# Kernel tuning notes

Measured on AMD Instinct MI355X. Metric: run time of the kernel, lower is better.

## Reference

```python
import jax, jax.numpy as jnp
import numpy as np


def setup_inputs() -> dict:
    key = jax.random.key(0)
    ks = jax.random.split(key, 8)
    d, h = 1024, 256
    bl, bh = 2048, 2048
    b = bl + bh
    w = lambda k, shp: jax.random.normal(k, shp, jnp.float32) * 0.02
    return {
        "z_low": jax.random.normal(ks[0], (bl, d), jnp.float32),
        "z_high": jax.random.normal(ks[1], (bh, d), jnp.float32),
        "z_bar": jax.random.normal(ks[2], (b, d), jnp.float32),
        "z_normal": jax.random.normal(ks[3], (b, d), jnp.float32),
        "Wa1": w(ks[4], (d, h)), "ba1": jnp.zeros((h,), jnp.float32),
        "Wa2": w(ks[5], (h,)), "ba2": jnp.zeros((), jnp.float32),
        "W0": w(ks[6], (d, d)), "b0": jnp.zeros((d,), jnp.float32),
        "W1": w(ks[7], (d, d)), "b1": jnp.zeros((d,), jnp.float32),
    }


def _scores(x, Wa1, ba1, Wa2, ba2):
    # Linear -> tanh -> Linear(->1); returns per-row attention logits [N]
    return jnp.tanh(x @ Wa1 + ba1) @ Wa2 + ba2


def _integrate(x, Wa1, ba1, Wa2, ba2):
    a = jax.nn.softmax(_scores(x, Wa1, ba1, Wa2, ba2))  # [N]
    return a @ x  # [dim]


def _loo_pool(x, Wa1, ba1, Wa2, ba2):
    # batched leave-one-out attention pooling: row i pools over all j != i
    n = x.shape[0]
    s = _scores(x, Wa1, ba1, Wa2, ba2)  # [N]
    S = jnp.broadcast_to(s[None, :], (n, n))
    S = jnp.where(jnp.eye(n, dtype=bool), -jnp.inf, S)
    A = jax.nn.softmax(S, axis=-1)  # [N,N], zero on diagonal
    return A @ x  # [N, dim]


def _cos(a, b, eps=1e-8):
    na = jnp.maximum(jnp.linalg.norm(a, axis=-1), eps)
    nb = jnp.maximum(jnp.linalg.norm(b, axis=-1), eps)
    return jnp.sum(a * b, axis=-1) / (na * nb)


def reference(z_low, z_high, z_bar, z_normal, Wa1, ba1, Wa2, ba2, W0, b0, W1, b1):
    z_all = jnp.concatenate([z_low, z_high], axis=0)  # [B, d]
    batch = z_all.shape[0]

    z_hat = jnp.concatenate([
        _loo_pool(z_low, Wa1, ba1, Wa2, ba2),
        _loo_pool(z_high, Wa1, ba1, Wa2, ba2),
    ], axis=0)  # [B, d]
    z_tumor = _loo_pool(z_all, Wa1, ba1, Wa2, ba2)  # [B, d]
    z_norm = _integrate(z_normal, Wa1, ba1, Wa2, ba2)  # [d]

    lin0 = lambda v: v @ W0 + b0
    lin1 = lambda v: v @ W1 + b1

    base = lin0(z_hat) + lin1(z_bar)
    pred_tumor = base + lin0(z_tumor)          # [B, d]
    pred_normal = base + lin0(z_norm)[None, :]  # [B, d]

    cpc_tumor = z_all @ pred_tumor.T    # [B, B]
    cpc_normal = z_all @ pred_normal.T  # [B, B]
    eye = jnp.eye(batch, dtype=cpc_tumor.dtype)
    total = eye * cpc_tumor + (1.0 - eye) * cpc_normal

    loss_tcl = jnp.sum(jnp.diag(jax.nn.log_softmax(total, axis=1))) / (-1.0 * batch)

    ones = jnp.ones((batch,), z_all.dtype)
    cos_loss = jnp.mean(ones - _cos(z_all, z_hat)) + jnp.mean(ones - _cos(z_all, z_bar))
    hinge_in = _cos(z_all, pred_tumor) - _cos(z_all, pred_normal)
    hinge = jnp.mean(jnp.maximum(0.0, 1.0 - hinge_in))  # HingeEmbeddingLoss, target=-1, margin=1
    loss_adc = cos_loss + hinge

    return (loss_tcl, loss_adc)
```

## Files before the change

### kernel.cpp

```cpp
#include <hip/hip_runtime.h>
#include <math.h>

#define D     1024
#define H     256
#define BLOW  2048
#define BTOT  4096
#define NCHUNK 64

using bf16x8 = __attribute__((ext_vector_type(8))) __bf16;
using f32x4  = __attribute__((ext_vector_type(4))) float;

static const size_t OFF_ZALL = 0;
static const size_t OFF_D2   = 4194304;
static const size_t T0       = 8388608;
static const size_t OFF_SALL = T0;
static const size_t OFF_SNORM= T0 + 4096;
static const size_t OFF_EGRP = T0 + 8192;
static const size_t OFF_ENORM= T0 + 16384;
static const size_t OFF_PLOW = T0 + 20480;
static const size_t OFF_PALL = T0 + 23552;
static const size_t OFF_ZNV  = T0 + 24576;
static const size_t OFF_WNORM= T0 + 25600;
static const size_t OFF_BIASC= T0 + 26624;
static const size_t OFF_STATS= T0 + 27648;
static const size_t OFF_ACC  = T0 + 27664;
static const size_t OFF_NZ   = T0 + 27680;
static const size_t OFF_DT   = T0 + 31776;
static const size_t OFF_G    = T0 + 35872;
static const size_t OFF_DIAG = T0 + 39968;
static const size_t OFF_PART = T0 + 44064;
static const size_t BF_BASE_F = 8972288;
static const size_t BF_ZALLN= 0;
static const size_t BF_ZCAT = 8388608;
static const size_t BF_ZTUM = 16777216;
static const size_t BF_C    = 20971520;
static const size_t BF_WCAT = 25165824;
static const size_t BF_WA1T = 27262976;

__device__ inline unsigned short f2bf(float f){
  unsigned u = __float_as_uint(f);
  u += 0x7fffu + ((u >> 16) & 1u);
  return (unsigned short)(u >> 16);
}
__device__ inline float bf2f(unsigned short u){
  return __uint_as_float(((unsigned)u) << 16);
}
__device__ inline float wave_sum(float v){
#pragma unroll
  for (int o = 32; o > 0; o >>= 1) v += __shfl_xor(v, o);
  return v;
}
__device__ inline float wave_maxf(float v){
#pragma unroll
  for (int o = 32; o > 0; o >>= 1) v = fmaxf(v, __shfl_xor(v, o));
  return v;
}
__device__ inline float block_sum(float v, float* sb){
  v = wave_sum(v);
  __syncthreads();
  if ((threadIdx.x & 63) == 0) sb[threadIdx.x >> 6] = v;
  __syncthreads();
  return sb[0] + sb[1] + sb[2] + sb[3];
}
__device__ inline float block_maxf(float v, float* sb){
  v = wave_maxf(v);
  __syncthreads();
  if ((threadIdx.x & 63) == 0) sb[threadIdx.x >> 6] = v;
  __syncthreads();
  return fmaxf(fmaxf(sb[0], sb[1]), fmaxf(sb[2], sb[3]));
}

__device__ inline void gload16(const unsigned short* g, unsigned short* l){
  __builtin_amdgcn_global_load_lds(
      (const __attribute__((address_space(1))) unsigned int*)g,
      (__attribute__((address_space(3))) unsigned int*)l, 16, 0, 0);
}

__global__ __launch_bounds__(256) void k_prep(const float* __restrict__ zl,
        const float* __restrict__ zh, const float* __restrict__ znorm,
        const float* __restrict__ zbar, float* __restrict__ za,
        unsigned short* __restrict__ zalln_bf, unsigned short* __restrict__ zcat_bf){
  int row = blockIdx.x, t = threadIdx.x, job = blockIdx.z;
  if (job == 0){
    const float4* src = (const float4*)((row < BLOW) ? (zl + (size_t)row * D)
                                                     : (zh + (size_t)(row - BLOW) * D));
    float4 v = src[t];
    ((float4*)(za + (size_t)row * D))[t] = v;
    *(ushort4*)(zalln_bf + (size_t)row * D + t * 4) =
        make_ushort4(f2bf(v.x), f2bf(v.y), f2bf(v.z), f2bf(v.w));
  } else if (job == 1){
    float4 v = ((const float4*)(znorm + (size_t)row * D))[t];
    *(ushort4*)(zalln_bf + (size_t)(BTOT + row) * D + t * 4) =
        make_ushort4(f2bf(v.x), f2bf(v.y), f2bf(v.z), f2bf(v.w));
  } else {
    float4 v = ((const float4*)(zbar + (size_t)row * D))[t];
    *(ushort4*)(zcat_bf + (size_t)row * 2048 + 1024 + t * 4) =
        make_ushort4(f2bf(v.x), f2bf(v.y), f2bf(v.z), f2bf(v.w));
  }
}

__global__ __launch_bounds__(256) void k_tconv3(const float* __restrict__ W0,
        const float* __restrict__ W1, const float* __restrict__ Wa1,
        unsigned short* __restrict__ WCAT, unsigned short* __restrict__ Wa1T){
  __shared__ float tile[32][33];
  int z = blockIdx.z;
  const float* in; unsigned short* out; int C, ostride;
  if (z == 0){ in = W0; out = WCAT; C = D; ostride = 2048; }
  else if (z == 1){ in = W1; out = WCAT + 1024; C = D; ostride = 2048; }
  else { if (blockIdx.x >= 8) return; in = Wa1; out = Wa1T; C = H; ostride = 1024; }
  int t = threadIdx.x;
  int lr = t >> 3;
  int lc = (t & 7) << 2;
  int gr = blockIdx.y * 32, gc = blockIdx.x * 32;
  float4 v = *(const float4*)(in + (size_t)(gr + lr) * C + gc + lc);
  tile[lr][lc + 0] = v.x; tile[lr][lc + 1] = v.y; tile[lr][lc + 2] = v.z; tile[lr][lc + 3] = v.w;
  __syncthreads();
  ushort4 o = make_ushort4(f2bf(tile[lc + 0][lr]), f2bf(tile[lc + 1][lr]),
                           f2bf(tile[lc + 2][lr]), f2bf(tile[lc + 3][lr]));
  *(ushort4*)(out + (size_t)(gc + lr) * ostride + gr + lc) = o;
}

__global__ __launch_bounds__(256) void k_zero13(float* __restrict__ ws){
  int i = blockIdx.x * 256 + threadIdx.x;
  if (i < 8192) ws[OFF_SALL + i] = 0.f;
  else if (i < 12288) ws[OFF_PLOW + i - 8192] = 0.f;
  else if (i < 13312) ws[OFF_WNORM + i - 12288] = 0.f;
  else if (i < 13328) ws[OFF_ACC + i - 13312] = 0.f;
}

__device__ inline void mfma_core_cv(const unsigned short* __restrict__ A, int sA,
                                    const unsigned short* __restrict__ B, int sB,
                                    int K, int row0, int col0,
                                    unsigned short* lds, f32x4 acc[4][4]){
  int t = threadIdx.x;
  int l = t & 63, w = t >> 6;
  int wrow = w >> 1, wcol = w & 1;
  int g = l >> 4, c15 = l & 15;
  const unsigned short* a0 = A + (size_t)(row0 + (t >> 2)) * sA + ((t & 3) << 3);
  const unsigned short* a1 = a0 + (size_t)64 * sA;
  const unsigned short* b0 = B + (size_t)(col0 + (t >> 2)) * sB + ((t & 3) << 3);
  const unsigned short* b1 = b0 + (size_t)64 * sB;
  int sd = w * 512;
  int abase = (wrow * 64 + c15) * 32 + g * 8;
  int bbase = 4096 + (wcol * 64 + c15) * 32 + g * 8;
  unsigned short* buf = lds;
  unsigned short* nxt = lds + 8192;
  gload16(a0, buf + sd);
  gload16(a1, buf + 2048 + sd);
  gload16(b0, buf + 4096 + sd);
  gload16(b1, buf + 6144 + sd);
  for (int kb = 0; kb < K; kb += 32){
    if (kb + 32 < K){
      gload16(a0 + kb + 32, nxt + sd);
      gload16(a1 + kb + 32, nxt + 2048 + sd);
      gload16(b0 + kb + 32, nxt + 4096 + sd);
      gload16(b1 + kb + 32, nxt + 6144 + sd);
      asm volatile("s_waitcnt vmcnt(4)" ::: "memory");
    } else {
      asm volatile("s_waitcnt vmcnt(0)" ::: "memory");
    }
    __builtin_amdgcn_sched_barrier(0);
    __builtin_amdgcn_s_barrier();
    __builtin_amdgcn_sched_barrier(0);
    bf16x8 af[4], bfr[4];
#pragma unroll
    for (int m = 0; m < 4; ++m) af[m]  = *(const bf16x8*)&buf[abase + m * 512];
#pragma unroll
    for (int n = 0; n < 4; ++n) bfr[n] = *(const bf16x8*)&buf[bbase + n * 512];
#pragma unroll
    for (int m = 0; m < 4; ++m)
#pragma unroll
      for (int n = 0; n < 4; ++n)
        acc[m][n] = __builtin_amdgcn_mfma_f32_16x16x32_bf16(af[m], bfr[n], acc[m][n], 0, 0, 0);
    __builtin_amdgcn_sched_barrier(0);
    __builtin_amdgcn_s_barrier();
    __builtin_amdgcn_sched_barrier(0);
    unsigned short* tmp = buf; buf = nxt; nxt = tmp;
  }
}

__global__ __launch_bounds__(256) void k_scores_bf(const unsigned short* __restrict__ Zbf,
        const unsigned short* __restrict__ Wa1T, const float* __restrict__ ba1,
        const float* __restrict__ Wa2, float* __restrict__ S){
  __shared__ __align__(16) unsigned short smem[16384];
  f32x4 acc[4][4];
  f32x4 zz = {0.f, 0.f, 0.f, 0.f};
#pragma unroll
  for (int m = 0; m < 4; ++m)
#pragma unroll
    for (int n = 0; n < 4; ++n) acc[m][n] = zz;
  int row0 = blockIdx.y * 128, col0 = blockIdx.x * 128;
  mfma_core_cv(Zbf, 1024, Wa1T, 1024, 1024, row0, col0, smem, acc);
  int t = threadIdx.x, l = t & 63, w = t >> 6, wrow = w >> 1, wcol = w & 1;
  int g = l >> 4, c15 = l & 15;
#pragma unroll
  for (int m = 0; m < 4; ++m){
#pragma unroll
    for (int r = 0; r < 4; ++r){
      float v = 0.f;
#pragma unroll
      for (int n = 0; n < 4; ++n){
        int col = col0 + wcol * 64 + n * 16 + c15;
        float x = acc[m][n][r] + ba1[col];
        float e = __expf(2.f * x);
        v += (1.f - 2.f / (e + 1.f)) * Wa2[col];
      }
      v += __shfl_xor(v, 1); v += __shfl_xor(v, 2); v += __shfl_xor(v, 4); v += __shfl_xor(v, 8);
      if (c15 == 0) atomicAdd(&S[row0 + wrow * 64 + m * 16 + 4 * g + r], v);
    }
  }
}

__global__ __launch_bounds__(256) void k_gemm_cd(const unsigned short* __restrict__ ZCAT,
        const unsigned short* __restrict__ ZTUM, const unsigned short* __restrict__ WCAT,
        const float* __restrict__ biasC, unsigned short* __restrict__ Cbf,
        float* __restrict__ D2){
  __shared__ __align__(16) unsigned short smem[16384];
  f32x4 acc[4][4];
  f32x4 zz = {0.f, 0.f, 0.f, 0.f};
#pragma unroll
  for (int m = 0; m < 4; ++m)
#pragma unroll
    for (int n = 0; n < 4; ++n) acc[m][n] = zz;
  int row0 = blockIdx.y * 128, col0 = blockIdx.x * 128;
  int t = threadIdx.x, l = t & 63, w = t >> 6, wrow = w >> 1, wcol = w & 1;
  int g = l >> 4, c15 = l & 15;
  if (blockIdx.z == 0){
    mfma_core_cv(ZCAT, 2048, WCAT, 2048, 2048, row0, col0, smem, acc);
#pragma unroll
    for (int m = 0; m < 4; ++m){
      int row = row0 + wrow * 64 + m * 16 + 4 * g;
#pragma unroll
      for (int n = 0; n < 4; ++n){
        int col = col0 + wcol * 64 + n * 16 + c15;
        float bv = biasC[col];
#pragma unroll
        for (int r = 0; r < 4; ++r)
          Cbf[(size_t)(row + r) * 1024 + col] = f2bf(acc[m][n][r] + bv);
      }
    }
  } else {
    mfma_core_cv(ZTUM, 1024, WCAT, 2048, 1024, row0, col0, smem, acc);
#pragma unroll
    for (int m = 0; m < 4; ++m){
      int row = row0 + wrow * 64 + m * 16 + 4 * g;
#pragma unroll
      for (int n = 0; n < 4; ++n){
        int col = col0 + wcol * 64 + n * 16 + c15;
#pragma unroll
        for (int r = 0; r < 4; ++r)
          D2[(size_t)(row + r) * 1024 + col] = acc[m][n][r];
      }
    }
  }
}

__global__ __launch_bounds__(256) void k_gemm_lse(const unsigned short* __restrict__ A,
        const unsigned short* __restrict__ B, float2* __restrict__ partials,
        float* __restrict__ diagM){
  __shared__ __align__(16) unsigned short smem[16384];
  f32x4 acc[4][4];
  f32x4 zz = {0.f, 0.f, 0.f, 0.f};
#pragma unroll
  for (int m = 0; m < 4; ++m)
#pragma unroll
    for (int n = 0; n < 4; ++n) acc[m][n] = zz;
  int row0 = blockIdx.y * 128, col0 = blockIdx.x * 128;
  mfma_core_cv(A, 1024, B, 1024, 1024, row0, col0, smem, acc);
  int t = threadIdx.x, l = t & 63, w = t >> 6, wrow = w >> 1, wcol = w & 1;
  int g = l >> 4, c15 = l & 15;
  int chunk = blockIdx.x * 2 + wcol;
#pragma unroll
  for (int m = 0; m < 4; ++m){
#pragma unroll
    for (int r = 0; r < 4; ++r){
      float lm = acc[m][0][r];
#pragma unroll
      for (int n = 1; n < 4; ++n) lm = fmaxf(lm, acc[m][n][r]);
      lm = fmaxf(lm, __shfl_xor(lm, 1));
      lm = fmaxf(lm, __shfl_xor(lm, 2));
      lm = fmaxf(lm, __shfl_xor(lm, 4));
      lm = fmaxf(lm, __shfl_xor(lm, 8));
      float ls = 0.f;
#pragma unroll
      for (int n = 0; n < 4; ++n) ls += __expf(acc[m][n][r] - lm);
      ls += __shfl_xor(ls, 1); ls += __shfl_xor(ls, 2); ls += __shfl_xor(ls, 4); ls += __shfl_xor(ls, 8);
      if (c15 == 0)
        partials[(size_t)chunk * BTOT + (row0 + wrow * 64 + m * 16 + 4 * g + r)] = make_float2(lm, ls);
    }
  }
  if (blockIdx.x == blockIdx.y && wrow == wcol && ((c15 >> 2) == g)){
#pragma unroll
    for (int m = 0; m < 4; ++m)
      diagM[row0 + wrow * 64 + m * 16 + c15] = acc[m][m][c15 & 3];
  }
}

__global__ __launch_bounds__(256) void k_stats(const float* __restrict__ s_all,
        const float* __restrict__ s_norm, float* __restrict__ e_grp,
        float* __restrict__ e_norm, float* __restrict__ stats){
  __shared__ float sb[4];
  int t = threadIdx.x;
  float va[16], vn[16];
#pragma unroll
  for (int j = 0; j < 16; ++j) va[j] = s_all[t + 256 * j];
#pragma unroll
  for (int j = 0; j < 16; ++j) vn[j] = s_norm[t + 256 * j];
  float m = -1e30f;
#pragma unroll
  for (int j = 0; j < 8; ++j) m = fmaxf(m, va[j]);
  float ml = block_maxf(m, sb);
  m = -1e30f;
#pragma unroll
  for (int j = 8; j < 16; ++j) m = fmaxf(m, va[j]);
  float mh = block_maxf(m, sb);
  m = -1e30f;
#pragma unroll
  for (int j = 0; j < 16; ++j) m = fmaxf(m, vn[j]);
  float mn = block_maxf(m, sb);
  float ma = fmaxf(ml, mh);
  float a = 0.f;
#pragma unroll
  for (int j = 0; j < 8; ++j){ float e = __expf(va[j] - ml); e_grp[t + 256 * j] = e; a += e; }
  float tl = block_sum(a, sb);
  a = 0.f;
#pragma unroll
  for (int j = 8; j < 16; ++j){ float e = __expf(va[j] - mh); e_grp[t + 256 * j] = e; a += e; }
  float th = block_sum(a, sb);
  a = 0.f;
#pragma unroll
  for (int j = 0; j < 16; ++j){ float e = __expf(vn[j] - mn); e_norm[t + 256 * j] = e; a += e; }
  float tn = block_sum(a, sb);
  if (t == 0){
    float sl = __expf(ml - ma), sh = __expf(mh - ma);
    stats[0] = ml; stats[1] = tl; stats[2] = mh; stats[3] = th;
    stats[4] = ma; stats[5] = tl * sl + th * sh; stats[6] = mn; stats[7] = tn;
    stats[8] = sl; stats[9] = sh;
  }
}

__global__ __launch_bounds__(256) void k_pvec(const float* __restrict__ z_all,
        const float* __restrict__ z_normal, const float* __restrict__ e_grp,
        const float* __restrict__ e_norm, float* __restrict__ P){
  int gz = blockIdx.z;
  const float* X; const float* E; float* Pg; int nr;
  if (gz == 0){ X = z_all;                         E = e_grp;        Pg = P;        nr = BLOW; }
  else if (gz == 1){ X = z_all + (size_t)BLOW * D; E = e_grp + BLOW; Pg = P + 1024; nr = BLOW; }
  else { X = z_normal;                             E = e_norm;       Pg = P + 2048; nr = BTOT; }
  int r0 = blockIdx.y * 16;
  if (r0 >= nr) return;
  int c4 = threadIdx.x * 4;
  float4 a = make_float4(0.f, 0.f, 0.f, 0.f);
#pragma unroll 4
  for (int r = r0; r < r0 + 16; ++r){
    float e = E[r];
    float4 x = *(const float4*)(X + (size_t)r * D + c4);
    a.x = fmaf(e, x.x, a.x); a.y = fmaf(e, x.y, a.y);
    a.z = fmaf(e, x.z, a.z); a.w = fmaf(e, x.w, a.w);
  }
  atomicAdd(&Pg[c4 + 0], a.x);
  atomicAdd(&Pg[c4 + 1], a.y);
  atomicAdd(&Pg[c4 + 2], a.z);
  atomicAdd(&Pg[c4 + 3], a.w);
}

__global__ __launch_bounds__(256) void k_smallvec(const float* __restrict__ P,
        const float* __restrict__ stats, const float* __restrict__ b0,
        const float* __restrict__ b1, float* __restrict__ P_all,
        float* __restrict__ znv, float* __restrict__ biasC){
  int c = blockIdx.x * 256 + threadIdx.x;
  znv[c] = P[2048 + c] / stats[7];
  biasC[c] = 2.f * b0[c] + b1[c];
  P_all[c] = stats[8] * P[c] + stats[9] * P[1024 + c];
}

__global__ __launch_bounds__(256) void k_wnorm(const float* __restrict__ znv,
        const float* __restrict__ W0, float* __restrict__ w_norm){
  int col = blockIdx.x * 256 + threadIdx.x;
  int kc = blockIdx.y;
  float a = 0.f;
  for (int k = kc * 128; k < kc * 128 + 128; ++k)
    a = fmaf(znv[k], W0[(size_t)k * D + col], a);
  atomicAdd(&w_norm[col], a);
}

__global__ __launch_bounds__(256) void k_zhat(const float* __restrict__ z_all,
        const float* __restrict__ z_bar, const float* __restrict__ e_grp,
        const float* __restrict__ stats,
        const float* __restrict__ P_low, const float* __restrict__ P_high,
        const float* __restrict__ P_all, unsigned short* __restrict__ zcat_bf,
        unsigned short* __restrict__ ztum_bf, float* __restrict__ nz_arr,
        float* __restrict__ accum){
  __shared__ float sb[4];
  int i = blockIdx.x, t = threadIdx.x;
  const float* Pg = (i < BLOW) ? P_low : P_high;
  float Tg = (i < BLOW) ? stats[1] : stats[3];
  float Ta = stats[5];
  float eg = e_grp[i];
  float ea = eg * ((i < BLOW) ? stats[8] : stats[9]);
  float ig = 1.f / (Tg - eg), ia = 1.f / (Ta - ea);
  size_t base = (size_t)i * D;
  float4 x  = ((const float4*)(z_all + base))[t];
  float4 pg = ((const float4*)Pg)[t];
  float4 pa = ((const float4*)P_all)[t];
  float4 zb = ((const float4*)(z_bar + base))[t];
  float4 zh, zt;
  zh.x = (pg.x - eg * x.x) * ig; zh.y = (pg.y - eg * x.y) * ig;
  zh.z = (pg.z - eg * x.z) * ig; zh.w = (pg.w - eg * x.w) * ig;
  zt.x = (pa.x - ea * x.x) * ia; zt.y = (pa.y - ea * x.y) * ia;
  zt.z = (pa.z - ea * x.z) * ia; zt.w = (pa.w - ea * x.w) * ia;
  *(ushort4*)(zcat_bf + (size_t)i * 2048 + t * 4) =
      make_ushort4(f2bf(zh.x), f2bf(zh.y), f2bf(zh.z), f2bf(zh.w));
  *(ushort4*)(ztum_bf + base + t * 4) = make_ushort4(f2bf(zt.x), f2bf(zt.y), f2bf(zt.z), f2bf(zt.w));
  float nz2 = x.x*x.x + x.y*x.y + x.z*x.z + x.w*x.w;
  float nh2 = zh.x*zh.x + zh.y*zh.y + zh.z*zh.z + zh.w*zh.w;
  float dzh = x.x*zh.x + x.y*zh.y + x.z*zh.z + x.w*zh.w;
  float nb2 = zb.x*zb.x + zb.y*zb.y + zb.z*zb.z + zb.w*zb.w;
  float dzb = x.x*zb.x + x.y*zb.y + x.z*zb.z + x.w*zb.w;
  float s_nz2 = block_sum(nz2, sb);
  float s_nh2 = block_sum(nh2, sb);
  float s_dzh = block_sum(dzh, sb);
  float s_nb2 = block_sum(nb2, sb);
  float s_dzb = block_sum(dzb, sb);
  if (t == 0){
    float nz = sqrtf(s_nz2);
    nz_arr[i] = nz;
    float denA = fmaxf(nz, 1e-8f) * fmaxf(sqrtf(s_nh2), 1e-8f);
    float denB = fmaxf(nz, 1e-8f) * fmaxf(sqrtf(s_nb2), 1e-8f);
    atomicAdd(&accum[0], (1.f - s_dzh / denA) + (1.f - s_dzb / denB));
  }
}

__global__ __launch_bounds__(256) void k_rowred2(const float* __restrict__ z_all,
        const float* __restrict__ D2, const unsigned short* __restrict__ Cbf,
        const float* __restrict__ w_norm, const float* __restrict__ nz_arr,
        float* __restrict__ dt_arr, float* __restrict__ g_arr, float* __restrict__ accum){
  __shared__ float sb[4];
  int i = blockIdx.x, t = threadIdx.x;
  size_t base = (size_t)i * D;
  float4 x  = ((const float4*)(z_all + base))[t];
  float4 d2 = ((const float4*)(D2 + base))[t];
  ushort4 cu = *(const ushort4*)(Cbf + base + t * 4);
  float4 c = make_float4(bf2f(cu.x), bf2f(cu.y), bf2f(cu.z), bf2f(cu.w));
  float4 wv = ((const float4*)w_norm)[t];
  float4 pt = make_float4(c.x + d2.x, c.y + d2.y, c.z + d2.z, c.w + d2.w);
  float4 pn = make_float4(c.x + wv.x, c.y + wv.y, c.z + wv.z, c.w + wv.w);
  float dt   = x.x*pt.x + x.y*pt.y + x.z*pt.z + x.w*pt.w;
  float npt2 = pt.x*pt.x + pt.y*pt.y + pt.z*pt.z + pt.w*pt.w;
  float dpn  = x.x*pn.x + x.y*pn.y + x.z*pn.z + x.w*pn.w;
  float npn2 = pn.x*pn.x + pn.y*pn.y + pn.z*pn.z + pn.w*pn.w;
  float gg   = x.x*wv.x + x.y*wv.y + x.z*wv.z + x.w*wv.w;
  float s_dt   = block_sum(dt, sb);
  float s_npt2 = block_sum(npt2, sb);
  float s_dpn  = block_sum(dpn, sb);
  float s_npn2 = block_sum(npn2, sb);
  float s_g    = block_sum(gg, sb);
  if (t == 0){
    dt_arr[i] = s_dt; g_arr[i] = s_g;
    float nz = fmaxf(nz_arr[i], 1e-8f);
    float ct = s_dt  / (nz * fmaxf(sqrtf(s_npt2), 1e-8f));
    float cn = s_dpn / (nz * fmaxf(sqrtf(s_npn2), 1e-8f));
    atomicAdd(&accum[1], fmaxf(0.f, 1.f - (ct - cn)));
  }
}

__global__ __launch_bounds__(256) void k_combine(const float2* __restrict__ partials,
        const float* __restrict__ diagM, const float* __restrict__ dt,
        const float* __restrict__ g, float* __restrict__ accum){
  __shared__ float sb[4];
  int i = blockIdx.x * 256 + threadIdx.x;
  float m = -1e30f, S = 0.f;
  for (int c = 0; c < NCHUNK; ++c){
    float2 p = partials[(size_t)c * BTOT + i];
    float nm = fmaxf(m, p.x);
    S = S * __expf(m - nm) + p.y * __expf(p.x - nm);
    m = nm;
  }
  float vold = diagM[i];
  float vnew = dt[i] - g[i];
  float nm = fmaxf(m, vnew);
  float S2 = S * __expf(m - nm) - __expf(vold - nm) + __expf(vnew - nm);
  float lse = g[i] + nm + logf(S2);
  float contrib = lse - dt[i];
  float tot = block_sum(contrib, sb);
  if (threadIdx.x == 0) atomicAdd(&accum[2], tot);
}

__global__ void k_final(const float* __restrict__ accum, float* __restrict__ out){
  out[0] = accum[2] / (float)BTOT;
  out[1] = (accum[0] + accum[1]) / (float)BTOT;
}

extern "C" void kernel_launch(void* const* d_in, const int* in_sizes, int n_in,
                              void* d_out, int out_size, void* d_ws, size_t ws_size,
                              hipStream_t stream){
  const float* z_low    = (const float*)d_in[0];
  const float* z_high   = (const float*)d_in[1];
  const float* z_bar    = (const float*)d_in[2];
  const float* z_normal = (const float*)d_in[3];
  const float* Wa1      = (const float*)d_in[4];
  const float* ba1      = (const float*)d_in[5];
  const float* Wa2      = (const float*)d_in[6];
  const float* ba2      = (const float*)d_in[7];
  const float* W0       = (const float*)d_in[8];
  const float* b0       = (const float*)d_in[9];
  const float* W1       = (const float*)d_in[10];
  const float* b1       = (const float*)d_in[11];
  float* ws = (float*)d_ws;
  unsigned short* bw = (unsigned short*)(ws + BF_BASE_F);
  float* out = (float*)d_out;
  (void)ba2;

  k_prep<<<dim3(BTOT, 1, 3), dim3(256), 0, stream>>>(z_low, z_high, z_normal, z_bar,
      ws + OFF_ZALL, bw + BF_ZALLN, bw + BF_ZCAT);
  k_tconv3<<<dim3(32, 32, 3), dim3(256), 0, stream>>>(W0, W1, Wa1,
      bw + BF_WCAT, bw + BF_WA1T);
  k_zero13<<<dim3(53), dim3(256), 0, stream>>>(ws);

  k_scores_bf<<<dim3(2, 64), dim3(256), 0, stream>>>(bw + BF_ZALLN, bw + BF_WA1T,
      ba1, Wa2, ws + OFF_SALL);

  k_stats<<<dim3(1), dim3(256), 0, stream>>>(ws + OFF_SALL, ws + OFF_SNORM,
      ws + OFF_EGRP, ws + OFF_ENORM, ws + OFF_STATS);

  k_pvec<<<dim3(1, 256, 3), dim3(256), 0, stream>>>(ws + OFF_ZALL, z_normal,
      ws + OFF_EGRP, ws + OFF_ENORM, ws + OFF_PLOW);

  k_smallvec<<<dim3(4), dim3(256), 0, stream>>>(ws + OFF_PLOW, ws + OFF_STATS,
      b0, b1, ws + OFF_PALL, ws + OFF_ZNV, ws + OFF_BIASC);

  k_wnorm<<<dim3(4, 8), dim3(256), 0, stream>>>(ws + OFF_ZNV, W0, ws + OFF_WNORM);

  k_zhat<<<dim3(BTOT), dim3(256), 0, stream>>>(ws + OFF_ZALL, z_bar,
      ws + OFF_EGRP, ws + OFF_STATS,
      ws + OFF_PLOW, ws + OFF_PLOW + 1024, ws + OFF_PALL,
      bw + BF_ZCAT, bw + BF_ZTUM, ws + OFF_NZ, ws + OFF_ACC);

  k_gemm_cd<<<dim3(8, 32, 2), dim3(256), 0, stream>>>(bw + BF_ZCAT, bw + BF_ZTUM,
      bw + BF_WCAT, ws + OFF_BIASC, bw + BF_C, ws + OFF_D2);

  k_rowred2<<<dim3(BTOT), dim3(256), 0, stream>>>(ws + OFF_ZALL, ws + OFF_D2,
      bw + BF_C, ws + OFF_WNORM, ws + OFF_NZ, ws + OFF_DT, ws + OFF_G, ws + OFF_ACC);

  k_gemm_lse<<<dim3(32, 32), dim3(256), 0, stream>>>(bw + BF_ZALLN, bw + BF_C,
      (float2*)(ws + OFF_PART), ws + OFF_DIAG);

  k_combine<<<dim3(16), dim3(256), 0, stream>>>((const float2*)(ws + OFF_PART),
      ws + OFF_DIAG, ws + OFF_DT, ws + OFF_G, ws + OFF_ACC);

  k_final<<<dim3(1), dim3(1), 0, stream>>>(ws + OFF_ACC, out);
}
```

Baseline: 388.1 us.

## Exploit linearity of leave-one-out pooling to replace concatenated GEMMs with Y=zW0, U=zbarW1

Leave-one-out pooled vectors are affine in each row (P - e·x)/(T - e), so lin0 of them is rewritten as per-row scalar combinations of Y = z_all·W0 and a few precomputed W0-projected vectors. The K=2048 concatenated GEMM and the extra K=1024 tumor GEMM become two independent K=1024 GEMMs, which can run before the score statistics are known. The zhat/rowred passes and the zeroing kernel are folded into a single fused row kernel and into the prep kernel, and the cos(z, z_hat) term is computed algebraically from ||P||². This trades GEMM FLOPs and intermediate traffic for extra bf16 rounding of Y, which is then scaled by possibly large per-row coefficients.

```diff
diff --git a/kernel.cpp b/kernel.cpp
--- a/kernel.cpp
+++ b/kernel.cpp
@@ -10,31 +10,26 @@
 using bf16x8 = __attribute__((ext_vector_type(8))) __bf16;
 using f32x4  = __attribute__((ext_vector_type(4))) float;
 
-static const size_t OFF_ZALL = 0;
-static const size_t OFF_D2   = 4194304;
-static const size_t T0       = 8388608;
-static const size_t OFF_SALL = T0;
-static const size_t OFF_SNORM= T0 + 4096;
-static const size_t OFF_EGRP = T0 + 8192;
-static const size_t OFF_ENORM= T0 + 16384;
-static const size_t OFF_PLOW = T0 + 20480;
-static const size_t OFF_PALL = T0 + 23552;
-static const size_t OFF_ZNV  = T0 + 24576;
-static const size_t OFF_WNORM= T0 + 25600;
-static const size_t OFF_BIASC= T0 + 26624;
-static const size_t OFF_STATS= T0 + 27648;
-static const size_t OFF_ACC  = T0 + 27664;
-static const size_t OFF_NZ   = T0 + 27680;
-static const size_t OFF_DT   = T0 + 31776;
-static const size_t OFF_G    = T0 + 35872;
-static const size_t OFF_DIAG = T0 + 39968;
-static const size_t OFF_PART = T0 + 44064;
-static const size_t BF_BASE_F = 8972288;
+static const size_t OFF_SALL = 0;
+static const size_t OFF_SNORM= 4096;
+static const size_t OFF_EGRP = 8192;
+static const size_t OFF_ENORM= 12288;
+static const size_t OFF_P    = 16384;
+static const size_t OFF_WV   = 19456;
+static const size_t OFF_STATS= 23552;
+static const size_t OFF_ACC  = 23568;
+static const size_t OFF_DT   = 23584;
+static const size_t OFF_G    = 27680;
+static const size_t OFF_DIAG = 31776;
+static const size_t OFF_PART = 35872;
+static const size_t BF_BASE_F = 560192;
 static const size_t BF_ZALLN= 0;
-static const size_t BF_ZCAT = 8388608;
-static const size_t BF_ZTUM = 16777216;
+static const size_t BF_ZBAR = 8388608;
+static const size_t BF_Y    = 12582912;
+static const size_t BF_U    = 16777216;
 static const size_t BF_C    = 20971520;
-static const size_t BF_WCAT = 25165824;
+static const size_t BF_W0T  = 25165824;
+static const size_t BF_W1T  = 26214400;
 static const size_t BF_WA1T = 27262976;
 
 __device__ inline unsigned short f2bf(float f){
@@ -78,36 +73,43 @@
 
 __global__ __launch_bounds__(256) void k_prep(const float* __restrict__ zl,
         const float* __restrict__ zh, const float* __restrict__ znorm,
-        const float* __restrict__ zbar, float* __restrict__ za,
-        unsigned short* __restrict__ zalln_bf, unsigned short* __restrict__ zcat_bf){
+        const float* __restrict__ zbar, float* __restrict__ ws,
+        unsigned short* __restrict__ zalln_bf, unsigned short* __restrict__ zbar_bf){
   int row = blockIdx.x, t = threadIdx.x, job = blockIdx.z;
   if (job == 0){
     const float4* src = (const float4*)((row < BLOW) ? (zl + (size_t)row * D)
                                                      : (zh + (size_t)(row - BLOW) * D));
     float4 v = src[t];
-    ((float4*)(za + (size_t)row * D))[t] = v;
     *(ushort4*)(zalln_bf + (size_t)row * D + t * 4) =
         make_ushort4(f2bf(v.x), f2bf(v.y), f2bf(v.z), f2bf(v.w));
   } else if (job == 1){
     float4 v = ((const float4*)(znorm + (size_t)row * D))[t];
     *(ushort4*)(zalln_bf + (size_t)(BTOT + row) * D + t * 4) =
         make_ushort4(f2bf(v.x), f2bf(v.y), f2bf(v.z), f2bf(v.w));
+    if (row < 61){
+      int i = row * 256 + t;
+      if (i < 8192) ws[OFF_SALL + i] = 0.f;
+      else if (i < 11264) ws[OFF_P + i - 8192] = 0.f;
+      else if (i < 15360) ws[OFF_WV + i - 11264] = 0.f;
+      else if (i < 15376) ws[OFF_ACC + i - 15360] = 0.f;
+    }
   } else {
     float4 v = ((const float4*)(zbar + (size_t)row * D))[t];
-    *(ushort4*)(zcat_bf + (size_t)row * 2048 + 1024 + t * 4) =
+    *(ushort4*)(zbar_bf + (size_t)row * D + t * 4) =
         make_ushort4(f2bf(v.x), f2bf(v.y), f2bf(v.z), f2bf(v.w));
   }
 }
 
 __global__ __launch_bounds__(256) void k_tconv3(const float* __restrict__ W0,
         const float* __restrict__ W1, const float* __restrict__ Wa1,
-        unsigned short* __restrict__ WCAT, unsigned short* __restrict__ Wa1T){
+        unsigned short* __restrict__ W0T, unsigned short* __restrict__ W1T,
+        unsigned short* __restrict__ Wa1T){
   __shared__ float tile[32][33];
   int z = blockIdx.z;
-  const float* in; unsigned short* out; int C, ostride;
-  if (z == 0){ in = W0; out = WCAT; C = D; ostride = 2048; }
-  else if (z == 1){ in = W1; out = WCAT + 1024; C = D; ostride = 2048; }
-  else { if (blockIdx.x >= 8) return; in = Wa1; out = Wa1T; C = H; ostride = 1024; }
+  const float* in; unsigned short* out; int C;
+  if (z == 0){ in = W0; out = W0T; C = D; }
+  else if (z == 1){ in = W1; out = W1T; C = D; }
+  else { if (blockIdx.x >= 8) return; in = Wa1; out = Wa1T; C = H; }
   int t = threadIdx.x;
   int lr = t >> 3;
   int lc = (t & 7) << 2;
@@ -117,15 +119,7 @@
   __syncthreads();
   ushort4 o = make_ushort4(f2bf(tile[lc + 0][lr]), f2bf(tile[lc + 1][lr]),
                            f2bf(tile[lc + 2][lr]), f2bf(tile[lc + 3][lr]));
-  *(ushort4*)(out + (size_t)(gc + lr) * ostride + gr + lc) = o;
-}
-
-__global__ __launch_bounds__(256) void k_zero13(float* __restrict__ ws){
-  int i = blockIdx.x * 256 + threadIdx.x;
-  if (i < 8192) ws[OFF_SALL + i] = 0.f;
-  else if (i < 12288) ws[OFF_PLOW + i - 8192] = 0.f;
-  else if (i < 13312) ws[OFF_WNORM + i - 12288] = 0.f;
-  else if (i < 13328) ws[OFF_ACC + i - 13312] = 0.f;
+  *(ushort4*)(out + (size_t)(gc + lr) * D + gr + lc) = o;
 }
 
 __device__ inline void mfma_core_cv(const unsigned short* __restrict__ A, int sA,
@@ -179,6 +173,37 @@
   }
 }
 
+__global__ __launch_bounds__(256) void k_gemm_yu(const unsigned short* __restrict__ ZALL,
+        const unsigned short* __restrict__ ZBAR, const unsigned short* __restrict__ W0T,
+        const unsigned short* __restrict__ W1T, unsigned short* __restrict__ Ybf,
+        unsigned short* __restrict__ Ubf){
+  __shared__ __align__(16) unsigned short smem[16384];
+  f32x4 acc[4][4];
+  f32x4 zz = {0.f, 0.f, 0.f, 0.f};
+#pragma unroll
+  for (int m = 0; m < 4; ++m)
+#pragma unroll
+    for (int n = 0; n < 4; ++n) acc[m][n] = zz;
+  int row0 = blockIdx.y * 128, col0 = blockIdx.x * 128;
+  const unsigned short* A = blockIdx.z ? ZBAR : ZALL;
+  const unsigned short* B = blockIdx.z ? W1T : W0T;
+  unsigned short* O = blockIdx.z ? Ubf : Ybf;
+  mfma_core_cv(A, 1024, B, 1024, 1024, row0, col0, smem, acc);
+  int t = threadIdx.x, l = t & 63, w = t >> 6, wrow = w >> 1, wcol = w & 1;
+  int g = l >> 4, c15 = l & 15;
+#pragma unroll
+  for (int m = 0; m < 4; ++m){
+    int row = row0 + wrow * 64 + m * 16 + 4 * g;
+#pragma unroll
+    for (int n = 0; n < 4; ++n){
+      int col = col0 + wcol * 64 + n * 16 + c15;
+#pragma unroll
+      for (int r = 0; r < 4; ++r)
+        O[(size_t)(row + r) * 1024 + col] = f2bf(acc[m][n][r]);
+    }
+  }
+}
+
 __global__ __launch_bounds__(256) void k_scores_bf(const unsigned short* __restrict__ Zbf,
         const unsigned short* __restrict__ Wa1T, const float* __restrict__ ba1,
         const float* __restrict__ Wa2, float* __restrict__ S){
@@ -211,50 +236,6 @@
   }
 }
 
-__global__ __launch_bounds__(256) void k_gemm_cd(const unsigned short* __restrict__ ZCAT,
-        const unsigned short* __restrict__ ZTUM, const unsigned short* __restrict__ WCAT,
-        const float* __restrict__ biasC, unsigned short* __restrict__ Cbf,
-        float* __restrict__ D2){
-  __shared__ __align__(16) unsigned short smem[16384];
-  f32x4 acc[4][4];
-  f32x4 zz = {0.f, 0.f, 0.f, 0.f};
-#pragma unroll
-  for (int m = 0; m < 4; ++m)
-#pragma unroll
-    for (int n = 0; n < 4; ++n) acc[m][n] = zz;
-  int row0 = blockIdx.y * 128, col0 = blockIdx.x * 128;
-  int t = threadIdx.x, l = t & 63, w = t >> 6, wrow = w >> 1, wcol = w & 1;
-  int g = l >> 4, c15 = l & 15;
-  if (blockIdx.z == 0){
-    mfma_core_cv(ZCAT, 2048, WCAT, 2048, 2048, row0, col0, smem, acc);
-#pragma unroll
-    for (int m = 0; m < 4; ++m){
-      int row = row0 + wrow * 64 + m * 16 + 4 * g;
-#pragma unroll
-      for (int n = 0; n < 4; ++n){
-        int col = col0 + wcol * 64 + n * 16 + c15;
-        float bv = biasC[col];
-#pragma unroll
-        for (int r = 0; r < 4; ++r)
-          Cbf[(size_t)(row + r) * 1024 + col] = f2bf(acc[m][n][r] + bv);
-      }
-    }
-  } else {
-    mfma_core_cv(ZTUM, 1024, WCAT, 2048, 1024, row0, col0, smem, acc);
-#pragma unroll
-    for (int m = 0; m < 4; ++m){
-      int row = row0 + wrow * 64 + m * 16 + 4 * g;
-#pragma unroll
-      for (int n = 0; n < 4; ++n){
-        int col = col0 + wcol * 64 + n * 16 + c15;
-#pragma unroll
-        for (int r = 0; r < 4; ++r)
-          D2[(size_t)(row + r) * 1024 + col] = acc[m][n][r];
-      }
-    }
-  }
-}
-
 __global__ __launch_bounds__(256) void k_gemm_lse(const unsigned short* __restrict__ A,
         const unsigned short* __restrict__ B, float2* __restrict__ partials,
         float* __restrict__ diagM){
@@ -335,18 +316,19 @@
     float sl = __expf(ml - ma), sh = __expf(mh - ma);
     stats[0] = ml; stats[1] = tl; stats[2] = mh; stats[3] = th;
     stats[4] = ma; stats[5] = tl * sl + th * sh; stats[6] = mn; stats[7] = tn;
-    stats[8] = sl; stats[9] = sh;
-  }
-}
-
-__global__ __launch_bounds__(256) void k_pvec(const float* __restrict__ z_all,
-        const float* __restrict__ z_normal, const float* __restrict__ e_grp,
-        const float* __restrict__ e_norm, float* __restrict__ P){
+    stats[8] = sl; stats[9] = sh; stats[10] = 0.f; stats[11] = 0.f;
+  }
+}
+
+__global__ __launch_bounds__(256) void k_pvec(const float* __restrict__ zl,
+        const float* __restrict__ zh, const float* __restrict__ znorm,
+        const float* __restrict__ e_grp, const float* __restrict__ e_norm,
+        float* __restrict__ P){
   int gz = blockIdx.z;
   const float* X; const float* E; float* Pg; int nr;
-  if (gz == 0){ X = z_all;                         E = e_grp;        Pg = P;        nr = BLOW; }
-  else if (gz == 1){ X = z_all + (size_t)BLOW * D; E = e_grp + BLOW; Pg = P + 1024; nr = BLOW; }
-  else { X = z_normal;                             E = e_norm;       Pg = P + 2048; nr = BTOT; }
+  if (gz == 0){ X = zl;       E = e_grp;        Pg = P;        nr = BLOW; }
+  else if (gz == 1){ X = zh;  E = e_grp + BLOW; Pg = P + 1024; nr = BLOW; }
+  else { X = znorm;           E = e_norm;       Pg = P + 2048; nr = BTOT; }
   int r0 = blockIdx.y * 16;
   if (r0 >= nr) return;
   int c4 = threadIdx.x * 4;
@@ -364,100 +346,103 @@
   atomicAdd(&Pg[c4 + 3], a.w);
 }
 
-__global__ __launch_bounds__(256) void k_smallvec(const float* __restrict__ P,
-        const float* __restrict__ stats, const float* __restrict__ b0,
-        const float* __restrict__ b1, float* __restrict__ P_all,
-        float* __restrict__ znv, float* __restrict__ biasC){
-  int c = blockIdx.x * 256 + threadIdx.x;
-  znv[c] = P[2048 + c] / stats[7];
-  biasC[c] = 2.f * b0[c] + b1[c];
-  P_all[c] = stats[8] * P[c] + stats[9] * P[1024 + c];
-}
-
-__global__ __launch_bounds__(256) void k_wnorm(const float* __restrict__ znv,
-        const float* __restrict__ W0, float* __restrict__ w_norm){
-  int col = blockIdx.x * 256 + threadIdx.x;
-  int kc = blockIdx.y;
+__global__ __launch_bounds__(256) void k_wvecs(const float* __restrict__ P,
+        float* __restrict__ stats, const float* __restrict__ W0, float* __restrict__ WV){
+  int t = threadIdx.x;
+  int col = blockIdx.x * 256 + t;
+  int k0 = blockIdx.y * 128;
+  int v = blockIdx.z;
+  float sl = stats[8], sh = stats[9], itn = 1.f / stats[7];
   float a = 0.f;
-  for (int k = kc * 128; k < kc * 128 + 128; ++k)
-    a = fmaf(znv[k], W0[(size_t)k * D + col], a);
-  atomicAdd(&w_norm[col], a);
-}
-
-__global__ __launch_bounds__(256) void k_zhat(const float* __restrict__ z_all,
-        const float* __restrict__ z_bar, const float* __restrict__ e_grp,
-        const float* __restrict__ stats,
-        const float* __restrict__ P_low, const float* __restrict__ P_high,
-        const float* __restrict__ P_all, unsigned short* __restrict__ zcat_bf,
-        unsigned short* __restrict__ ztum_bf, float* __restrict__ nz_arr,
-        float* __restrict__ accum){
+  for (int k = k0; k < k0 + 128; ++k){
+    float coeff = (v == 0) ? P[k]
+                : (v == 1) ? P[1024 + k]
+                : (v == 2) ? sl * P[k] + sh * P[1024 + k]
+                : P[2048 + k] * itn;
+    a = fmaf(coeff, W0[(size_t)k * D + col], a);
+  }
+  atomicAdd(&WV[v * 1024 + col], a);
+  if (v < 2 && blockIdx.x == 0){
+    __shared__ float sb[4];
+    float s = 0.f;
+    if (t < 128){ float pv = P[v * 1024 + k0 + t]; s = pv * pv; }
+    s = block_sum(s, sb);
+    if (t == 0) atomicAdd(&stats[10 + v], s);
+  }
+}
+
+__global__ __launch_bounds__(256) void k_fuse(const float* __restrict__ zl,
+        const float* __restrict__ zh, const float* __restrict__ zbar,
+        const unsigned short* __restrict__ Ybf, const unsigned short* __restrict__ Ubf,
+        const float* __restrict__ e_grp, const float* __restrict__ stats,
+        const float* __restrict__ P, const float* __restrict__ WV,
+        const float* __restrict__ b0, const float* __restrict__ b1,
+        unsigned short* __restrict__ Cbf, float* __restrict__ dt_arr,
+        float* __restrict__ g_arr, float* __restrict__ accum){
   __shared__ float sb[4];
   int i = blockIdx.x, t = threadIdx.x;
-  const float* Pg = (i < BLOW) ? P_low : P_high;
-  float Tg = (i < BLOW) ? stats[1] : stats[3];
-  float Ta = stats[5];
+  bool lo = i < BLOW;
+  const float* zrow = lo ? zl + (size_t)i * D : zh + (size_t)(i - BLOW) * D;
   float eg = e_grp[i];
-  float ea = eg * ((i < BLOW) ? stats[8] : stats[9]);
-  float ig = 1.f / (Tg - eg), ia = 1.f / (Ta - ea);
+  float Tg = lo ? stats[1] : stats[3];
+  float sg = lo ? stats[8] : stats[9];
+  float PP = lo ? stats[10] : stats[11];
+  float ea = eg * sg, Ta = stats[5];
+  float ag = 1.f / (Tg - eg), bg = -eg * ag;
+  float aa = 1.f / (Ta - ea), ba = -ea * aa;
+  const float* Pg = lo ? P : P + 1024;
+  const float* wg = lo ? WV : WV + 1024;
   size_t base = (size_t)i * D;
-  float4 x  = ((const float4*)(z_all + base))[t];
-  float4 pg = ((const float4*)Pg)[t];
-  float4 pa = ((const float4*)P_all)[t];
-  float4 zb = ((const float4*)(z_bar + base))[t];
-  float4 zh, zt;
-  zh.x = (pg.x - eg * x.x) * ig; zh.y = (pg.y - eg * x.y) * ig;
-  zh.z = (pg.z - eg * x.z) * ig; zh.w = (pg.w - eg * x.w) * ig;
-  zt.x = (pa.x - ea * x.x) * ia; zt.y = (pa.y - ea * x.y) * ia;
-  zt.z = (pa.z - ea * x.z) * ia; zt.w = (pa.w - ea * x.w) * ia;
-  *(ushort4*)(zcat_bf + (size_t)i * 2048 + t * 4) =
-      make_ushort4(f2bf(zh.x), f2bf(zh.y), f2bf(zh.z), f2bf(zh.w));
-  *(ushort4*)(ztum_bf + base + t * 4) = make_ushort4(f2bf(zt.x), f2bf(zt.y), f2bf(zt.z), f2bf(zt.w));
-  float nz2 = x.x*x.x + x.y*x.y + x.z*x.z + x.w*x.w;
-  float nh2 = zh.x*zh.x + zh.y*zh.y + zh.z*zh.z + zh.w*zh.w;
-  float dzh = x.x*zh.x + x.y*zh.y + x.z*zh.z + x.w*zh.w;
-  float nb2 = zb.x*zb.x + zb.y*zb.y + zb.z*zb.z + zb.w*zb.w;
-  float dzb = x.x*zb.x + x.y*zb.y + x.z*zb.z + x.w*zb.w;
-  float s_nz2 = block_sum(nz2, sb);
-  float s_nh2 = block_sum(nh2, sb);
-  float s_dzh = block_sum(dzh, sb);
-  float s_nb2 = block_sum(nb2, sb);
-  float s_dzb = block_sum(dzb, sb);
-  if (t == 0){
-    float nz = sqrtf(s_nz2);
-    nz_arr[i] = nz;
-    float denA = fmaxf(nz, 1e-8f) * fmaxf(sqrtf(s_nh2), 1e-8f);
-    float denB = fmaxf(nz, 1e-8f) * fmaxf(sqrtf(s_nb2), 1e-8f);
-    atomicAdd(&accum[0], (1.f - s_dzh / denA) + (1.f - s_dzb / denB));
-  }
-}
-
-__global__ __launch_bounds__(256) void k_rowred2(const float* __restrict__ z_all,
-        const float* __restrict__ D2, const unsigned short* __restrict__ Cbf,
-        const float* __restrict__ w_norm, const float* __restrict__ nz_arr,
-        float* __restrict__ dt_arr, float* __restrict__ g_arr, float* __restrict__ accum){
-  __shared__ float sb[4];
-  int i = blockIdx.x, t = threadIdx.x;
-  size_t base = (size_t)i * D;
-  float4 x  = ((const float4*)(z_all + base))[t];
-  float4 d2 = ((const float4*)(D2 + base))[t];
-  ushort4 cu = *(const ushort4*)(Cbf + base + t * 4);
-  float4 c = make_float4(bf2f(cu.x), bf2f(cu.y), bf2f(cu.z), bf2f(cu.w));
-  float4 wv = ((const float4*)w_norm)[t];
-  float4 pt = make_float4(c.x + d2.x, c.y + d2.y, c.z + d2.z, c.w + d2.w);
-  float4 pn = make_float4(c.x + wv.x, c.y + wv.y, c.z + wv.z, c.w + wv.w);
-  float dt   = x.x*pt.x + x.y*pt.y + x.z*pt.z + x.w*pt.w;
+  float4 x   = ((const float4*)zrow)[t];
+  float4 zb  = ((const float4*)(zbar + base))[t];
+  ushort4 y4 = *(const ushort4*)(Ybf + base + t * 4);
+  ushort4 u4 = *(const ushort4*)(Ubf + base + t * 4);
+  float4 y = make_float4(bf2f(y4.x), bf2f(y4.y), bf2f(y4.z), bf2f(y4.w));
+  float4 u = make_float4(bf2f(u4.x), bf2f(u4.y), bf2f(u4.z), bf2f(u4.w));
+  float4 pg4 = ((const float4*)Pg)[t];
+  float4 wg4 = ((const float4*)wg)[t];
+  float4 wa4 = ((const float4*)(WV + 2048))[t];
+  float4 wn4 = ((const float4*)(WV + 3072))[t];
+  float4 b04 = ((const float4*)b0)[t];
+  float4 b14 = ((const float4*)b1)[t];
+  float4 c;
+  c.x = fmaf(ag, wg4.x, fmaf(bg, y.x, u.x + 2.f * b04.x + b14.x));
+  c.y = fmaf(ag, wg4.y, fmaf(bg, y.y, u.y + 2.f * b04.y + b14.y));
+  c.z = fmaf(ag, wg4.z, fmaf(bg, y.z, u.z + 2.f * b04.z + b14.z));
+  c.w = fmaf(ag, wg4.w, fmaf(bg, y.w, u.w + 2.f * b04.w + b14.w));
+  *(ushort4*)(Cbf + base + t * 4) = make_ushort4(f2bf(c.x), f2bf(c.y), f2bf(c.z), f2bf(c.w));
+  float4 pt;
+  pt.x = c.x + fmaf(aa, wa4.x, ba * y.x);
+  pt.y = c.y + fmaf(aa, wa4.y, ba * y.y);
+  pt.z = c.z + fmaf(aa, wa4.z, ba * y.z);
+  pt.w = c.w + fmaf(aa, wa4.w, ba * y.w);
+  float4 pn = make_float4(c.x + wn4.x, c.y + wn4.y, c.z + wn4.z, c.w + wn4.w);
+  float nz2  = x.x*x.x + x.y*x.y + x.z*x.z + x.w*x.w;
+  float zPg  = x.x*pg4.x + x.y*pg4.y + x.z*pg4.z + x.w*pg4.w;
+  float nb2  = zb.x*zb.x + zb.y*zb.y + zb.z*zb.z + zb.w*zb.w;
+  float dzb  = x.x*zb.x + x.y*zb.y + x.z*zb.z + x.w*zb.w;
+  float dtv  = x.x*pt.x + x.y*pt.y + x.z*pt.z + x.w*pt.w;
   float npt2 = pt.x*pt.x + pt.y*pt.y + pt.z*pt.z + pt.w*pt.w;
   float dpn  = x.x*pn.x + x.y*pn.y + x.z*pn.z + x.w*pn.w;
   float npn2 = pn.x*pn.x + pn.y*pn.y + pn.z*pn.z + pn.w*pn.w;
-  float gg   = x.x*wv.x + x.y*wv.y + x.z*wv.z + x.w*wv.w;
-  float s_dt   = block_sum(dt, sb);
+  float gg   = x.x*wn4.x + x.y*wn4.y + x.z*wn4.z + x.w*wn4.w;
+  float s_nz2  = block_sum(nz2, sb);
+  float s_zPg  = block_sum(zPg, sb);
+  float s_nb2  = block_sum(nb2, sb);
+  float s_dzb  = block_sum(dzb, sb);
+  float s_dt   = block_sum(dtv, sb);
   float s_npt2 = block_sum(npt2, sb);
   float s_dpn  = block_sum(dpn, sb);
   float s_npn2 = block_sum(npn2, sb);
   float s_g    = block_sum(gg, sb);
   if (t == 0){
     dt_arr[i] = s_dt; g_arr[i] = s_g;
-    float nz = fmaxf(nz_arr[i], 1e-8f);
+    float nz = fmaxf(sqrtf(s_nz2), 1e-8f);
+    float dzh = ag * (s_zPg - eg * s_nz2);
+    float nh2 = ag * ag * (PP - 2.f * eg * s_zPg + eg * eg * s_nz2);
+    float cosA = dzh / (nz * fmaxf(sqrtf(nh2), 1e-8f));
+    float cosB = s_dzb / (nz * fmaxf(sqrtf(s_nb2), 1e-8f));
+    atomicAdd(&accum[0], (1.f - cosA) + (1.f - cosB));
     float ct = s_dt  / (nz * fmaxf(sqrtf(s_npt2), 1e-8f));
     float cn = s_dpn / (nz * fmaxf(sqrtf(s_npn2), 1e-8f));
     atomicAdd(&accum[1], fmaxf(0.f, 1.f - (ct - cn)));
@@ -512,10 +497,12 @@
   (void)ba2;
 
   k_prep<<<dim3(BTOT, 1, 3), dim3(256), 0, stream>>>(z_low, z_high, z_normal, z_bar,
-      ws + OFF_ZALL, bw + BF_ZALLN, bw + BF_ZCAT);
+      ws, bw + BF_ZALLN, bw + BF_ZBAR);
   k_tconv3<<<dim3(32, 32, 3), dim3(256), 0, stream>>>(W0, W1, Wa1,
-      bw + BF_WCAT, bw + BF_WA1T);
-  k_zero13<<<dim3(53), dim3(256), 0, stream>>>(ws);
+      bw + BF_W0T, bw + BF_W1T, bw + BF_WA1T);
+
+  k_gemm_yu<<<dim3(8, 32, 2), dim3(256), 0, stream>>>(bw + BF_ZALLN, bw + BF_ZBAR,
+      bw + BF_W0T, bw + BF_W1T, bw + BF_Y, bw + BF_U);
 
   k_scores_bf<<<dim3(2, 64), dim3(256), 0, stream>>>(bw + BF_ZALLN, bw + BF_WA1T,
       ba1, Wa2, ws + OFF_SALL);
@@ -523,24 +510,15 @@
   k_stats<<<dim3(1), dim3(256), 0, stream>>>(ws + OFF_SALL, ws + OFF_SNORM,
       ws + OFF_EGRP, ws + OFF_ENORM, ws + OFF_STATS);
 
-  k_pvec<<<dim3(1, 256, 3), dim3(256), 0, stream>>>(ws + OFF_ZALL, z_normal,
-      ws + OFF_EGRP, ws + OFF_ENORM, ws + OFF_PLOW);
-
-  k_smallvec<<<dim3(4), dim3(256), 0, stream>>>(ws + OFF_PLOW, ws + OFF_STATS,
-      b0, b1, ws + OFF_PALL, ws + OFF_ZNV, ws + OFF_BIASC);
-
-  k_wnorm<<<dim3(4, 8), dim3(256), 0, stream>>>(ws + OFF_ZNV, W0, ws + OFF_WNORM);
-
-  k_zhat<<<dim3(BTOT), dim3(256), 0, stream>>>(ws + OFF_ZALL, z_bar,
-      ws + OFF_EGRP, ws + OFF_STATS,
-      ws + OFF_PLOW, ws + OFF_PLOW + 1024, ws + OFF_PALL,
-      bw + BF_ZCAT, bw + BF_ZTUM, ws + OFF_NZ, ws + OFF_ACC);
-
-  k_gemm_cd<<<dim3(8, 32, 2), dim3(256), 0, stream>>>(bw + BF_ZCAT, bw + BF_ZTUM,
-      bw + BF_WCAT, ws + OFF_BIASC, bw + BF_C, ws + OFF_D2);
-
-  k_rowred2<<<dim3(BTOT), dim3(256), 0, stream>>>(ws + OFF_ZALL, ws + OFF_D2,
-      bw + BF_C, ws + OFF_WNORM, ws + OFF_NZ, ws + OFF_DT, ws + OFF_G, ws + OFF_ACC);
+  k_pvec<<<dim3(1, 256, 3), dim3(256), 0, stream>>>(z_low, z_high, z_normal,
+      ws + OFF_EGRP, ws + OFF_ENORM, ws + OFF_P);
+
+  k_wvecs<<<dim3(4, 8, 4), dim3(256), 0, stream>>>(ws + OFF_P, ws + OFF_STATS,
+      W0, ws + OFF_WV);
+
+  k_fuse<<<dim3(BTOT), dim3(256), 0, stream>>>(z_low, z_high, z_bar,
+      bw + BF_Y, bw + BF_U, ws + OFF_EGRP, ws + OFF_STATS, ws + OFF_P, ws + OFF_WV,
+      b0, b1, bw + BF_C, ws + OFF_DT, ws + OFF_G, ws + OFF_ACC);
 
   k_gemm_lse<<<dim3(32, 32), dim3(256), 0, stream>>>(bw + BF_ZALLN, bw + BF_C,
       (float2*)(ws + OFF_PART), ws + OFF_DIAG);
```

Result: no change. 389.1 us (+0.3%).
